# Kernel tuning notes

Hardware: AMD Instinct MI355X
Metric: run time of the kernel (lower is better)

Reference implementation:

```python
import jax, jax.numpy as jnp
import numpy as np

BATCH, SEQ, N_INPUT, N_HIDDEN, N_OUTPUT = 256, 512, 512, 128, 2


def setup_inputs() -> dict:
    key = jax.random.key(0)
    ks = jax.random.split(key, 6)
    s_i = 1.0 / np.sqrt(N_INPUT)
    s_h = 1.0 / np.sqrt(N_HIDDEN)
    return {
        "x": jax.random.normal(ks[0], (BATCH, SEQ, N_INPUT), dtype=jnp.float32),
        # LSTM gate kernels, gate order (i, f, g, o) concatenated on last axis.
        # flax nn.LSTMCell: dense_i has no bias, dense_h has bias.
        "Wi": jax.random.normal(ks[1], (N_INPUT, 4 * N_HIDDEN), dtype=jnp.float32) * s_i,
        "Wh": jax.random.normal(ks[2], (N_HIDDEN, 4 * N_HIDDEN), dtype=jnp.float32) * s_h,
        "b": jax.random.normal(ks[3], (4 * N_HIDDEN,), dtype=jnp.float32) * 0.01,
        "Wd": jax.random.normal(ks[4], (N_HIDDEN, N_OUTPUT), dtype=jnp.float32) * s_h,
        "bd": jax.random.normal(ks[5], (N_OUTPUT,), dtype=jnp.float32) * 0.01,
    }


def reference(x, Wi, Wh, b, Wd, bd):
    B, S, _ = x.shape
    H = Wh.shape[0]
    # Precompute input projection for all steps in one big GEMM: (S, B, 4H)
    x_gates = jnp.einsum('bsi,ig->sbg', x, Wi)

    def step(carry, xg):
        c, h = carry
        gates = xg + h @ Wh + b  # (B, 4H)
        i, f, g, o = jnp.split(gates, 4, axis=-1)
        c = jax.nn.sigmoid(f) * c + jax.nn.sigmoid(i) * jnp.tanh(g)
        h = jax.nn.sigmoid(o) * jnp.tanh(c)
        return (c, h), h

    c0 = jnp.zeros((B, H), dtype=x.dtype)
    h0 = jnp.zeros((B, H), dtype=x.dtype)
    (_, h_last), _ = jax.lax.scan(step, (c0, h0), x_gates)
    logits = h_last @ Wd + bd  # (B, N_OUTPUT)
    return logits
```

## Files before the change

### kernel.cpp

```cpp
#include <hip/hip_runtime.h>
#include <hip/hip_bf16.h>


typedef __attribute__((ext_vector_type(8))) short short8;
typedef __attribute__((ext_vector_type(4))) float floatx4;
typedef __attribute__((ext_vector_type(4))) unsigned short ushortx4;
typedef __attribute__((ext_vector_type(2))) unsigned int uint2v;

#define LOG2E 1.44269504088896340736f

__device__ __forceinline__ unsigned short f2bf(float f) {
  unsigned int u = __builtin_bit_cast(unsigned int, f);
  u = (u + 0x7fffu + ((u >> 16) & 1u)) >> 16;
  return (unsigned short)u;
}
__device__ __forceinline__ float bf2f(unsigned short u) {
  unsigned int v = ((unsigned int)u) << 16;
  return __builtin_bit_cast(float, v);
}
__device__ __forceinline__ float sigf(float x) {
  return __builtin_amdgcn_rcpf(1.0f + __builtin_amdgcn_exp2f(-LOG2E * x));
}
__device__ __forceinline__ float tanhf_(float x) {
  return 1.0f - 2.0f * __builtin_amdgcn_rcpf(1.0f + __builtin_amdgcn_exp2f(2.0f * LOG2E * x));
}
__device__ __forceinline__ void bar_lds() {
  asm volatile("s_waitcnt lgkmcnt(0)" ::: "memory");
  __builtin_amdgcn_s_barrier();
  __builtin_amdgcn_sched_barrier(0);
}
__device__ __forceinline__ void gl_lds16(const void* g, void* l) {
  __builtin_amdgcn_global_load_lds(
      (const __attribute__((address_space(1))) unsigned int*)g,
      (__attribute__((address_space(3))) unsigned int*)l, 16, 0, 0);
}

__global__ void pack_kernel(const float* __restrict__ Wi, const float* __restrict__ Wh,
                            unsigned short* __restrict__ Wi_p, unsigned short* __restrict__ Wh_p) {
  int idx = blockIdx.x * 256 + threadIdx.x;
  if (idx < 262144) {
    int j = idx & 7, lane = (idx >> 3) & 63, nt = (idx >> 9) & 31, kk = idx >> 14;
    int k = kk * 32 + ((lane >> 4) * 8) + j;
    int n = nt * 16 + (lane & 15);
    Wi_p[idx] = f2bf(Wi[k * 512 + n]);
  } else {
    int i2 = idx - 262144;
    int j = i2 & 7, lane = (i2 >> 3) & 63, nt = (i2 >> 9) & 31, kk = i2 >> 14;
    int k = kk * 32 + ((lane >> 4) * 8) + j;
    int n = nt * 16 + (lane & 15);
    Wh_p[i2] = f2bf(Wh[k * 512 + n]);
  }
}

__global__ __launch_bounds__(512, 2) void xgemm_kernel(
    const float* __restrict__ x, const unsigned short* __restrict__ Wi_p,
    const float* __restrict__ bias, unsigned int* __restrict__ xg5) {
  __shared__ __align__(16) unsigned short As[128 * 72];
  __shared__ __align__(16) unsigned short Bs[2 * 32 * 64 * 8];

  const int tid = threadIdx.x;
  const int lane = tid & 63;
  const int w = tid >> 6;
  const int wm = w >> 2, wn = w & 3;
  const int quad = lane >> 4;
  const int lm = lane & 15;
  const int bm = blockIdx.x;
  const int s = bm >> 1;
  const int b0 = (bm & 1) * 128;

  float bs_[4][2];
  #pragma unroll
  for (int g = 0; g < 4; ++g)
    #pragma unroll
    for (int jc = 0; jc < 2; ++jc)
      bs_[g][jc] = bias[g * 128 + wn * 32 + jc * 16 + lm];

  floatx4 acc[4][8];
  #pragma unroll
  for (int a = 0; a < 4; ++a)
    #pragma unroll
    for (int b2 = 0; b2 < 8; ++b2) { acc[a][b2].x = 0.f; acc[a][b2].y = 0.f; acc[a][b2].z = 0.f; acc[a][b2].w = 0.f; }

  const float* xbase = x + ((size_t)(b0 + w * 16 + quad) * 512 + s) * 512 + lm * 4;

  floatx4 cur[4], nxt[4];
  #pragma unroll
  for (int i = 0; i < 4; ++i)
    cur[i] = *(const floatx4*)(xbase + (size_t)i * 1048576);

  for (int kt = 0; kt < 8; ++kt) {
    bar_lds();
    #pragma unroll
    for (int i = 0; i < 4; ++i) {
      int r = w * 16 + i * 4 + quad;
      ushortx4 u;
      u.x = f2bf(cur[i].x); u.y = f2bf(cur[i].y); u.z = f2bf(cur[i].z); u.w = f2bf(cur[i].w);
      *(ushortx4*)(&As[r * 72 + lm * 4]) = u;
    }
    #pragma unroll
    for (int c = 0; c < 8; ++c) {
      int kg = c & 1, ntl = (c >> 1) * 8 + w;
      const unsigned short* src = Wi_p + ((size_t)((kt * 2 + kg) * 32 + ntl) * 64 + lane) * 8;
      unsigned short* dst = &Bs[(size_t)((kg * 32 + ntl) * 64) * 8];
      gl_lds16(src, dst);
    }
    __builtin_amdgcn_sched_barrier(0);
    if (kt < 7) {
      #pragma unroll
      for (int i = 0; i < 4; ++i)
        nxt[i] = *(const floatx4*)(xbase + (size_t)i * 1048576 + (kt + 1) * 64);
      asm volatile("s_waitcnt vmcnt(4) lgkmcnt(0)" ::: "memory");
    } else {
      asm volatile("s_waitcnt vmcnt(0) lgkmcnt(0)" ::: "memory");
    }
    __builtin_amdgcn_s_barrier();
    __builtin_amdgcn_sched_barrier(0);
    #pragma unroll
    for (int ks = 0; ks < 2; ++ks) {
      short8 af[4];
      #pragma unroll
      for (int mt = 0; mt < 4; ++mt) {
        int m = wm * 64 + mt * 16 + lm;
        af[mt] = *(const short8*)(&As[m * 72 + ks * 32 + quad * 8]);
      }
      #pragma unroll
      for (int nt = 0; nt < 8; ++nt) {
        int g = nt >> 1, jc = nt & 1;
        int ntl = g * 8 + wn * 2 + jc;
        short8 bfv = *(const short8*)(&Bs[(size_t)((ks * 32 + ntl) * 64 + lane) * 8]);
        #pragma unroll
        for (int mt = 0; mt < 4; ++mt)
          acc[mt][nt] = __builtin_amdgcn_mfma_f32_16x16x32_bf16(af[mt], bfv, acc[mt][nt], 0, 0, 0);
      }
    }
    #pragma unroll
    for (int i = 0; i < 4; ++i) cur[i] = nxt[i];
  }
  #pragma unroll
  for (int mt = 0; mt < 4; ++mt) {
    int bbase = b0 + wm * 64 + mt * 16 + quad * 4;
    #pragma unroll
    for (int jc = 0; jc < 2; ++jc) {
      int wv = wn * 2 + jc;
      #pragma unroll
      for (int rr = 0; rr < 4; ++rr) {
        size_t cell = ((size_t)s * 64 + ((bbase + rr) >> 2)) * 512 + wv * 64 + rr * 16 + lm;
        float g0 = acc[mt][0 + jc][rr] + bs_[0][jc];
        float g1 = acc[mt][2 + jc][rr] + bs_[1][jc];
        float g2 = acc[mt][4 + jc][rr] + bs_[2][jc];
        float g3 = acc[mt][6 + jc][rr] + bs_[3][jc];
        uint2v v;
        v.x = (unsigned int)f2bf(g0) | ((unsigned int)f2bf(g1) << 16);
        v.y = (unsigned int)f2bf(g2) | ((unsigned int)f2bf(g3) << 16);
        *(uint2v*)(xg5 + cell * 2) = v;
      }
    }
  }
}

__global__ __launch_bounds__(512, 2) void lstm_kernel(
    const unsigned int* __restrict__ xg5, const unsigned short* __restrict__ Wh_p,
    const float* __restrict__ Wd, const float* __restrict__ bd,
    float* __restrict__ out) {
  __shared__ __align__(16) unsigned short hb[2 * 16 * 140];
  __shared__ __align__(16) float gbw[8 * 320];

  const int tid = threadIdx.x;
  const int lane = tid & 63;
  const int w = tid >> 6;
  const int quad = lane >> 4;
  const int lm = lane & 15;
  const int bb = blockIdx.x;

  for (int i = tid; i < 2 * 16 * 140; i += 512) hb[i] = 0;

  short8 bfr[4][4];
  #pragma unroll
  for (int kk = 0; kk < 4; ++kk)
    #pragma unroll
    for (int g = 0; g < 4; ++g)
      bfr[kk][g] = *(const short8*)(Wh_p + ((size_t)(kk * 32 + g * 8 + w) * 64 + lane) * 8);

  float cst = 0.f;

  const unsigned int* xp = xg5 + ((size_t)bb * 512 + tid) * 2;
  uint2v xga = *(const uint2v*)(xp);
  uint2v xgb = *(const uint2v*)(xp + 65536);

  float* gw = gbw + w * 320;

  __syncthreads();

  auto substep = [&](const int rp, uint2v& xcur, int spre) {
    uint2v xv = xcur;
    if (spre < 512)
      xcur = *(const uint2v*)(xp + (size_t)spre * 65536);

    short8 af[4];
    #pragma unroll
    for (int kk = 0; kk < 4; ++kk) {
      const unsigned short* p = &hb[rp * 2240 + lm * 140 + kk * 32 + quad * 8];
      union { short8 v; ushortx4 h[2]; } t;
      t.h[0] = *(const ushortx4*)(p);
      t.h[1] = *(const ushortx4*)(p + 4);
      af[kk] = t.v;
    }
    floatx4 acc[4];
    #pragma unroll
    for (int g = 0; g < 4; ++g) { acc[g].x = 0.f; acc[g].y = 0.f; acc[g].z = 0.f; acc[g].w = 0.f; }
    #pragma unroll
    for (int kk = 0; kk < 4; ++kk)
      #pragma unroll
      for (int g = 0; g < 4; ++g)
        acc[g] = __builtin_amdgcn_mfma_f32_16x16x32_bf16(af[kk], bfr[kk][g], acc[g], 0, 0, 0);

    if (lane < 16) {
      #pragma unroll
      for (int r = 0; r < 4; ++r) {
        floatx4 t4;
        t4.x = acc[0][r]; t4.y = acc[1][r]; t4.z = acc[2][r]; t4.w = acc[3][r];
        *(floatx4*)(gw + lm * 20 + r * 4) = t4;
      }
    }
    asm volatile("s_waitcnt lgkmcnt(0)" ::: "memory");
    __builtin_amdgcn_sched_barrier(0);
    floatx4 gv = *(const floatx4*)(gw + lm * 20 + quad * 4);

    float pre0 = gv.x + bf2f((unsigned short)(xv.x & 0xffffu));
    float pre1 = gv.y + bf2f((unsigned short)(xv.x >> 16));
    float pre2 = gv.z + bf2f((unsigned short)(xv.y & 0xffffu));
    float pre3 = gv.w + bf2f((unsigned short)(xv.y >> 16));
    float cc = sigf(pre1) * cst + sigf(pre0) * tanhf_(pre2);
    cst = cc;
    float hv = sigf(pre3) * tanhf_(cc);
    hb[(rp ^ 1) * 2240 + quad * 140 + w * 16 + lm] = f2bf(hv);
    bar_lds();
  };

  for (int s = 0; s < 512; s += 2) {
    substep(0, xga, s + 2);
    substep(1, xgb, s + 3);
  }

  if (tid < 8) {
    int rw = tid >> 1, co = tid & 1;
    float a = bd[co];
    for (int j2 = 0; j2 < 128; ++j2)
      a += bf2f(hb[rw * 140 + j2]) * Wd[j2 * 2 + co];
    out[(bb * 4 + rw) * 2 + co] = a;
  }
}

extern "C" void kernel_launch(void* const* d_in, const int* in_sizes, int n_in,
                              void* d_out, int out_size, void* d_ws, size_t ws_size,
                              hipStream_t stream) {
  const float* x  = (const float*)d_in[0];
  const float* Wi = (const float*)d_in[1];
  const float* Wh = (const float*)d_in[2];
  const float* b  = (const float*)d_in[3];
  const float* Wd = (const float*)d_in[4];
  const float* bd = (const float*)d_in[5];
  float* out = (float*)d_out;

  unsigned short* Wi_p = (unsigned short*)d_ws;
  unsigned short* Wh_p = Wi_p + 262144;
  unsigned int*   xg5  = (unsigned int*)(Wh_p + 65536);

  pack_kernel<<<1280, 256, 0, stream>>>(Wi, Wh, Wi_p, Wh_p);
  xgemm_kernel<<<1024, 512, 0, stream>>>(x, Wi_p, b, xg5);
  lstm_kernel<<<64, 512, 0, stream>>>(xg5, Wh_p, Wd, bd, out);
}
```

Before: 755.9 us.

## Fuse input GEMM and LSTM recurrence into one kernel with chunked flag handoff

Merges the input-projection GEMM and the recurrent LSTM kernel into a single persistent launch. 192 blocks run the GEMM over timestep chunks and bump per-chunk atomic counters, while 64 blocks run the recurrence and spin on those counters before consuming each 64-step chunk. The goal is to overlap the bandwidth-bound GEMM with the latency-bound serial recurrence instead of running them back to back. This relies on all 256 blocks being co-resident to avoid deadlock, and the GEMM blocks compete with the recurrence blocks for memory and CU resources.

```diff
diff --git a/kernel.cpp b/kernel.cpp
--- a/kernel.cpp
+++ b/kernel.cpp
@@ -36,7 +36,9 @@
 }
 
 __global__ void pack_kernel(const float* __restrict__ Wi, const float* __restrict__ Wh,
-                            unsigned short* __restrict__ Wi_p, unsigned short* __restrict__ Wh_p) {
+                            unsigned short* __restrict__ Wi_p, unsigned short* __restrict__ Wh_p,
+                            unsigned int* __restrict__ flags) {
+  if (blockIdx.x == 0 && threadIdx.x < 8) flags[threadIdx.x] = 0u;
   int idx = blockIdx.x * 256 + threadIdx.x;
   if (idx < 262144) {
     int j = idx & 7, lane = (idx >> 3) & 63, nt = (idx >> 9) & 31, kk = idx >> 14;
@@ -52,116 +54,14 @@
   }
 }
 
-__global__ __launch_bounds__(512, 2) void xgemm_kernel(
+__global__ __launch_bounds__(512, 2) void fused_kernel(
     const float* __restrict__ x, const unsigned short* __restrict__ Wi_p,
-    const float* __restrict__ bias, unsigned int* __restrict__ xg5) {
+    const float* __restrict__ bias, unsigned int* __restrict__ xg5,
+    const unsigned short* __restrict__ Wh_p, const float* __restrict__ Wd,
+    const float* __restrict__ bd, float* __restrict__ out,
+    unsigned int* __restrict__ flags) {
   __shared__ __align__(16) unsigned short As[128 * 72];
   __shared__ __align__(16) unsigned short Bs[2 * 32 * 64 * 8];
-
-  const int tid = threadIdx.x;
-  const int lane = tid & 63;
-  const int w = tid >> 6;
-  const int wm = w >> 2, wn = w & 3;
-  const int quad = lane >> 4;
-  const int lm = lane & 15;
-  const int bm = blockIdx.x;
-  const int s = bm >> 1;
-  const int b0 = (bm & 1) * 128;
-
-  float bs_[4][2];
-  #pragma unroll
-  for (int g = 0; g < 4; ++g)
-    #pragma unroll
-    for (int jc = 0; jc < 2; ++jc)
-      bs_[g][jc] = bias[g * 128 + wn * 32 + jc * 16 + lm];
-
-  floatx4 acc[4][8];
-  #pragma unroll
-  for (int a = 0; a < 4; ++a)
-    #pragma unroll
-    for (int b2 = 0; b2 < 8; ++b2) { acc[a][b2].x = 0.f; acc[a][b2].y = 0.f; acc[a][b2].z = 0.f; acc[a][b2].w = 0.f; }
-
-  const float* xbase = x + ((size_t)(b0 + w * 16 + quad) * 512 + s) * 512 + lm * 4;
-
-  floatx4 cur[4], nxt[4];
-  #pragma unroll
-  for (int i = 0; i < 4; ++i)
-    cur[i] = *(const floatx4*)(xbase + (size_t)i * 1048576);
-
-  for (int kt = 0; kt < 8; ++kt) {
-    bar_lds();
-    #pragma unroll
-    for (int i = 0; i < 4; ++i) {
-      int r = w * 16 + i * 4 + quad;
-      ushortx4 u;
-      u.x = f2bf(cur[i].x); u.y = f2bf(cur[i].y); u.z = f2bf(cur[i].z); u.w = f2bf(cur[i].w);
-      *(ushortx4*)(&As[r * 72 + lm * 4]) = u;
-    }
-    #pragma unroll
-    for (int c = 0; c < 8; ++c) {
-      int kg = c & 1, ntl = (c >> 1) * 8 + w;
-      const unsigned short* src = Wi_p + ((size_t)((kt * 2 + kg) * 32 + ntl) * 64 + lane) * 8;
-      unsigned short* dst = &Bs[(size_t)((kg * 32 + ntl) * 64) * 8];
-      gl_lds16(src, dst);
-    }
-    __builtin_amdgcn_sched_barrier(0);
-    if (kt < 7) {
-      #pragma unroll
-      for (int i = 0; i < 4; ++i)
-        nxt[i] = *(const floatx4*)(xbase + (size_t)i * 1048576 + (kt + 1) * 64);
-      asm volatile("s_waitcnt vmcnt(4) lgkmcnt(0)" ::: "memory");
-    } else {
-      asm volatile("s_waitcnt vmcnt(0) lgkmcnt(0)" ::: "memory");
-    }
-    __builtin_amdgcn_s_barrier();
-    __builtin_amdgcn_sched_barrier(0);
-    #pragma unroll
-    for (int ks = 0; ks < 2; ++ks) {
-      short8 af[4];
-      #pragma unroll
-      for (int mt = 0; mt < 4; ++mt) {
-        int m = wm * 64 + mt * 16 + lm;
-        af[mt] = *(const short8*)(&As[m * 72 + ks * 32 + quad * 8]);
-      }
-      #pragma unroll
-      for (int nt = 0; nt < 8; ++nt) {
-        int g = nt >> 1, jc = nt & 1;
-        int ntl = g * 8 + wn * 2 + jc;
-        short8 bfv = *(const short8*)(&Bs[(size_t)((ks * 32 + ntl) * 64 + lane) * 8]);
-        #pragma unroll
-        for (int mt = 0; mt < 4; ++mt)
-          acc[mt][nt] = __builtin_amdgcn_mfma_f32_16x16x32_bf16(af[mt], bfv, acc[mt][nt], 0, 0, 0);
-      }
-    }
-    #pragma unroll
-    for (int i = 0; i < 4; ++i) cur[i] = nxt[i];
-  }
-  #pragma unroll
-  for (int mt = 0; mt < 4; ++mt) {
-    int bbase = b0 + wm * 64 + mt * 16 + quad * 4;
-    #pragma unroll
-    for (int jc = 0; jc < 2; ++jc) {
-      int wv = wn * 2 + jc;
-      #pragma unroll
-      for (int rr = 0; rr < 4; ++rr) {
-        size_t cell = ((size_t)s * 64 + ((bbase + rr) >> 2)) * 512 + wv * 64 + rr * 16 + lm;
-        float g0 = acc[mt][0 + jc][rr] + bs_[0][jc];
-        float g1 = acc[mt][2 + jc][rr] + bs_[1][jc];
-        float g2 = acc[mt][4 + jc][rr] + bs_[2][jc];
-        float g3 = acc[mt][6 + jc][rr] + bs_[3][jc];
-        uint2v v;
-        v.x = (unsigned int)f2bf(g0) | ((unsigned int)f2bf(g1) << 16);
-        v.y = (unsigned int)f2bf(g2) | ((unsigned int)f2bf(g3) << 16);
-        *(uint2v*)(xg5 + cell * 2) = v;
-      }
-    }
-  }
-}
-
-__global__ __launch_bounds__(512, 2) void lstm_kernel(
-    const unsigned int* __restrict__ xg5, const unsigned short* __restrict__ Wh_p,
-    const float* __restrict__ Wd, const float* __restrict__ bd,
-    float* __restrict__ out) {
   __shared__ __align__(16) unsigned short hb[2 * 16 * 140];
   __shared__ __align__(16) float gbw[8 * 320];
 
@@ -170,84 +70,197 @@
   const int w = tid >> 6;
   const int quad = lane >> 4;
   const int lm = lane & 15;
-  const int bb = blockIdx.x;
-
-  for (int i = tid; i < 2 * 16 * 140; i += 512) hb[i] = 0;
-
-  short8 bfr[4][4];
-  #pragma unroll
-  for (int kk = 0; kk < 4; ++kk)
+
+  if (blockIdx.x < 192) {
+    const int wm = w >> 2, wn = w & 3;
+
+    float bs_[4][2];
     #pragma unroll
     for (int g = 0; g < 4; ++g)
-      bfr[kk][g] = *(const short8*)(Wh_p + ((size_t)(kk * 32 + g * 8 + w) * 64 + lane) * 8);
-
-  float cst = 0.f;
-
-  const unsigned int* xp = xg5 + ((size_t)bb * 512 + tid) * 2;
-  uint2v xga = *(const uint2v*)(xp);
-  uint2v xgb = *(const uint2v*)(xp + 65536);
-
-  float* gw = gbw + w * 320;
-
-  __syncthreads();
-
-  auto substep = [&](const int rp, uint2v& xcur, int spre) {
-    uint2v xv = xcur;
-    if (spre < 512)
-      xcur = *(const uint2v*)(xp + (size_t)spre * 65536);
-
-    short8 af[4];
-    #pragma unroll
-    for (int kk = 0; kk < 4; ++kk) {
-      const unsigned short* p = &hb[rp * 2240 + lm * 140 + kk * 32 + quad * 8];
-      union { short8 v; ushortx4 h[2]; } t;
-      t.h[0] = *(const ushortx4*)(p);
-      t.h[1] = *(const ushortx4*)(p + 4);
-      af[kk] = t.v;
+      #pragma unroll
+      for (int jc = 0; jc < 2; ++jc)
+        bs_[g][jc] = bias[g * 128 + wn * 32 + jc * 16 + lm];
+
+    for (int t = blockIdx.x; t < 1024; t += 192) {
+      const int s = t >> 1;
+      const int b0 = (t & 1) * 128;
+
+      floatx4 acc[4][8];
+      #pragma unroll
+      for (int a = 0; a < 4; ++a)
+        #pragma unroll
+        for (int b2 = 0; b2 < 8; ++b2) { acc[a][b2].x = 0.f; acc[a][b2].y = 0.f; acc[a][b2].z = 0.f; acc[a][b2].w = 0.f; }
+
+      const float* xbase = x + ((size_t)(b0 + w * 16 + quad) * 512 + s) * 512 + lm * 4;
+
+      floatx4 cur[4], nxt[4];
+      #pragma unroll
+      for (int i = 0; i < 4; ++i)
+        cur[i] = *(const floatx4*)(xbase + (size_t)i * 1048576);
+
+      for (int kt = 0; kt < 8; ++kt) {
+        bar_lds();
+        #pragma unroll
+        for (int i = 0; i < 4; ++i) {
+          int r = w * 16 + i * 4 + quad;
+          ushortx4 u;
+          u.x = f2bf(cur[i].x); u.y = f2bf(cur[i].y); u.z = f2bf(cur[i].z); u.w = f2bf(cur[i].w);
+          *(ushortx4*)(&As[r * 72 + lm * 4]) = u;
+        }
+        #pragma unroll
+        for (int c = 0; c < 8; ++c) {
+          int kg = c & 1, ntl = (c >> 1) * 8 + w;
+          const unsigned short* src = Wi_p + ((size_t)((kt * 2 + kg) * 32 + ntl) * 64 + lane) * 8;
+          unsigned short* dst = &Bs[(size_t)((kg * 32 + ntl) * 64) * 8];
+          gl_lds16(src, dst);
+        }
+        __builtin_amdgcn_sched_barrier(0);
+        if (kt < 7) {
+          #pragma unroll
+          for (int i = 0; i < 4; ++i)
+            nxt[i] = *(const floatx4*)(xbase + (size_t)i * 1048576 + (kt + 1) * 64);
+          asm volatile("s_waitcnt vmcnt(4) lgkmcnt(0)" ::: "memory");
+        } else {
+          asm volatile("s_waitcnt vmcnt(0) lgkmcnt(0)" ::: "memory");
+        }
+        __builtin_amdgcn_s_barrier();
+        __builtin_amdgcn_sched_barrier(0);
+        #pragma unroll
+        for (int ks = 0; ks < 2; ++ks) {
+          short8 af[4];
+          #pragma unroll
+          for (int mt = 0; mt < 4; ++mt) {
+            int m = wm * 64 + mt * 16 + lm;
+            af[mt] = *(const short8*)(&As[m * 72 + ks * 32 + quad * 8]);
+          }
+          #pragma unroll
+          for (int nt = 0; nt < 8; ++nt) {
+            int g = nt >> 1, jc = nt & 1;
+            int ntl = g * 8 + wn * 2 + jc;
+            short8 bfv = *(const short8*)(&Bs[(size_t)((ks * 32 + ntl) * 64 + lane) * 8]);
+            #pragma unroll
+            for (int mt = 0; mt < 4; ++mt)
+              acc[mt][nt] = __builtin_amdgcn_mfma_f32_16x16x32_bf16(af[mt], bfv, acc[mt][nt], 0, 0, 0);
+          }
+        }
+        #pragma unroll
+        for (int i = 0; i < 4; ++i) cur[i] = nxt[i];
+      }
+      #pragma unroll
+      for (int mt = 0; mt < 4; ++mt) {
+        int bbase = b0 + wm * 64 + mt * 16 + quad * 4;
+        #pragma unroll
+        for (int jc = 0; jc < 2; ++jc) {
+          int wv = wn * 2 + jc;
+          #pragma unroll
+          for (int rr = 0; rr < 4; ++rr) {
+            size_t cell = ((size_t)s * 64 + ((bbase + rr) >> 2)) * 512 + wv * 64 + rr * 16 + lm;
+            float g0 = acc[mt][0 + jc][rr] + bs_[0][jc];
+            float g1 = acc[mt][2 + jc][rr] + bs_[1][jc];
+            float g2 = acc[mt][4 + jc][rr] + bs_[2][jc];
+            float g3 = acc[mt][6 + jc][rr] + bs_[3][jc];
+            uint2v v;
+            v.x = (unsigned int)f2bf(g0) | ((unsigned int)f2bf(g1) << 16);
+            v.y = (unsigned int)f2bf(g2) | ((unsigned int)f2bf(g3) << 16);
+            *(uint2v*)(xg5 + cell * 2) = v;
+          }
+        }
+      }
+      __syncthreads();
+      if (tid == 0)
+        __hip_atomic_fetch_add(&flags[t >> 7], 1u, __ATOMIC_RELEASE, __HIP_MEMORY_SCOPE_AGENT);
     }
-    floatx4 acc[4];
-    #pragma unroll
-    for (int g = 0; g < 4; ++g) { acc[g].x = 0.f; acc[g].y = 0.f; acc[g].z = 0.f; acc[g].w = 0.f; }
+  } else {
+    const int bb = blockIdx.x - 192;
+
+    for (int i = tid; i < 2 * 16 * 140; i += 512) hb[i] = 0;
+
+    short8 bfr[4][4];
     #pragma unroll
     for (int kk = 0; kk < 4; ++kk)
       #pragma unroll
       for (int g = 0; g < 4; ++g)
-        acc[g] = __builtin_amdgcn_mfma_f32_16x16x32_bf16(af[kk], bfr[kk][g], acc[g], 0, 0, 0);
-
-    if (lane < 16) {
-      #pragma unroll
-      for (int r = 0; r < 4; ++r) {
-        floatx4 t4;
-        t4.x = acc[0][r]; t4.y = acc[1][r]; t4.z = acc[2][r]; t4.w = acc[3][r];
-        *(floatx4*)(gw + lm * 20 + r * 4) = t4;
+        bfr[kk][g] = *(const short8*)(Wh_p + ((size_t)(kk * 32 + g * 8 + w) * 64 + lane) * 8);
+
+    float cst = 0.f;
+
+    const unsigned int* xp = xg5 + ((size_t)bb * 512 + tid) * 2;
+    float* gw = gbw + w * 320;
+
+    while (__hip_atomic_load(&flags[0], __ATOMIC_ACQUIRE, __HIP_MEMORY_SCOPE_AGENT) < 128u)
+      __builtin_amdgcn_s_sleep(2);
+
+    uint2v xga = *(const uint2v*)(xp);
+    uint2v xgb = *(const uint2v*)(xp + 65536);
+
+    __syncthreads();
+
+    auto substep = [&](const int rp, uint2v& xcur, int spre) {
+      uint2v xv = xcur;
+      if (spre < 512)
+        xcur = *(const uint2v*)(xp + (size_t)spre * 65536);
+
+      short8 af[4];
+      #pragma unroll
+      for (int kk = 0; kk < 4; ++kk) {
+        const unsigned short* p = &hb[rp * 2240 + lm * 140 + kk * 32 + quad * 8];
+        union { short8 v; ushortx4 h[2]; } t;
+        t.h[0] = *(const ushortx4*)(p);
+        t.h[1] = *(const ushortx4*)(p + 4);
+        af[kk] = t.v;
+      }
+      floatx4 acc[4];
+      #pragma unroll
+      for (int g = 0; g < 4; ++g) { acc[g].x = 0.f; acc[g].y = 0.f; acc[g].z = 0.f; acc[g].w = 0.f; }
+      #pragma unroll
+      for (int kk = 0; kk < 4; ++kk)
+        #pragma unroll
+        for (int g = 0; g < 4; ++g)
+          acc[g] = __builtin_amdgcn_mfma_f32_16x16x32_bf16(af[kk], bfr[kk][g], acc[g], 0, 0, 0);
+
+      if (lane < 16) {
+        #pragma unroll
+        for (int r = 0; r < 4; ++r) {
+          floatx4 t4;
+          t4.x = acc[0][r]; t4.y = acc[1][r]; t4.z = acc[2][r]; t4.w = acc[3][r];
+          *(floatx4*)(gw + lm * 20 + r * 4) = t4;
+        }
+      }
+      asm volatile("s_waitcnt lgkmcnt(0)" ::: "memory");
+      __builtin_amdgcn_sched_barrier(0);
+      floatx4 gv = *(const floatx4*)(gw + lm * 20 + quad * 4);
+
+      float pre0 = gv.x + bf2f((unsigned short)(xv.x & 0xffffu));
+      float pre1 = gv.y + bf2f((unsigned short)(xv.x >> 16));
+      float pre2 = gv.z + bf2f((unsigned short)(xv.y & 0xffffu));
+      float pre3 = gv.w + bf2f((unsigned short)(xv.y >> 16));
+      float cc = sigf(pre1) * cst + sigf(pre0) * tanhf_(pre2);
+      cst = cc;
+      float hv = sigf(pre3) * tanhf_(cc);
+      hb[(rp ^ 1) * 2240 + quad * 140 + w * 16 + lm] = f2bf(hv);
+      bar_lds();
+    };
+
+    for (int c = 0; c < 8; ++c) {
+      if (c < 7) {
+        while (__hip_atomic_load(&flags[c + 1], __ATOMIC_ACQUIRE, __HIP_MEMORY_SCOPE_AGENT) < 128u)
+          __builtin_amdgcn_s_sleep(2);
+      }
+      #pragma unroll 1
+      for (int s2 = 0; s2 < 64; s2 += 2) {
+        int s = c * 64 + s2;
+        substep(0, xga, s + 2);
+        substep(1, xgb, s + 3);
       }
     }
-    asm volatile("s_waitcnt lgkmcnt(0)" ::: "memory");
-    __builtin_amdgcn_sched_barrier(0);
-    floatx4 gv = *(const floatx4*)(gw + lm * 20 + quad * 4);
-
-    float pre0 = gv.x + bf2f((unsigned short)(xv.x & 0xffffu));
-    float pre1 = gv.y + bf2f((unsigned short)(xv.x >> 16));
-    float pre2 = gv.z + bf2f((unsigned short)(xv.y & 0xffffu));
-    float pre3 = gv.w + bf2f((unsigned short)(xv.y >> 16));
-    float cc = sigf(pre1) * cst + sigf(pre0) * tanhf_(pre2);
-    cst = cc;
-    float hv = sigf(pre3) * tanhf_(cc);
-    hb[(rp ^ 1) * 2240 + quad * 140 + w * 16 + lm] = f2bf(hv);
-    bar_lds();
-  };
-
-  for (int s = 0; s < 512; s += 2) {
-    substep(0, xga, s + 2);
-    substep(1, xgb, s + 3);
-  }
-
-  if (tid < 8) {
-    int rw = tid >> 1, co = tid & 1;
-    float a = bd[co];
-    for (int j2 = 0; j2 < 128; ++j2)
-      a += bf2f(hb[rw * 140 + j2]) * Wd[j2 * 2 + co];
-    out[(bb * 4 + rw) * 2 + co] = a;
+
+    if (tid < 8) {
+      int rw = tid >> 1, co = tid & 1;
+      float a = bd[co];
+      for (int j2 = 0; j2 < 128; ++j2)
+        a += bf2f(hb[rw * 140 + j2]) * Wd[j2 * 2 + co];
+      out[(bb * 4 + rw) * 2 + co] = a;
+    }
   }
 }
 
@@ -264,9 +277,9 @@
 
   unsigned short* Wi_p = (unsigned short*)d_ws;
   unsigned short* Wh_p = Wi_p + 262144;
-  unsigned int*   xg5  = (unsigned int*)(Wh_p + 65536);
-
-  pack_kernel<<<1280, 256, 0, stream>>>(Wi, Wh, Wi_p, Wh_p);
-  xgemm_kernel<<<1024, 512, 0, stream>>>(x, Wi_p, b, xg5);
-  lstm_kernel<<<64, 512, 0, stream>>>(xg5, Wh_p, Wd, bd, out);
-}
+  unsigned int*   flags = (unsigned int*)(Wh_p + 65536);
+  unsigned int*   xg5  = flags + 128;
+
+  pack_kernel<<<1280, 256, 0, stream>>>(Wi, Wh, Wi_p, Wh_p, flags);
+  fused_kernel<<<256, 512, 0, stream>>>(x, Wi_p, b, xg5, Wh_p, Wd, bd, out, flags);
+}
```

New measurement: 798.8 us. 1.06x slower.
